# Performance work log

Measured on AMD Instinct MI355X. Metric: run time of the kernel, lower is better.

Reference implementation:

```python
import jax, jax.numpy as jnp
import numpy as np

B, T, P, D, S, R = 4, 128, 256, 512, 64, 8  # batch, window, patches, d_model, n_state, dt_rank


def setup_inputs() -> dict:
    key = jax.random.key(0)
    ks = jax.random.split(key, 8)
    sc = 0.02  # weight init scale
    return {
        "X": jax.random.normal(ks[0], (B, T, P, D), jnp.float32),
        "H0": jnp.zeros((B, P, S), jnp.float32),
        "a_hat": jax.random.normal(ks[1], (S,), jnp.float32),
        "U_w": jax.random.normal(ks[2], (S, D), jnp.float32) * sc,
        "sB_w": jax.random.normal(ks[3], (S, D), jnp.float32) * sc,
        "sB_b": jnp.zeros((S,), jnp.float32),
        "sC_w": jax.random.normal(ks[4], (S, D), jnp.float32) * sc,
        "sC_b": jnp.zeros((S,), jnp.float32),
        "sD1_w": jax.random.normal(ks[5], (R, D), jnp.float32) * sc,
        "sD1_b": jnp.zeros((R,), jnp.float32),
        "sD2_w": jax.random.normal(ks[6], (1, R), jnp.float32) * sc,
        "sD2_b": jnp.zeros((1,), jnp.float32),
        "ro_w": jax.random.normal(ks[7], (D, S), jnp.float32) * sc,
    }


def reference(X, H0, a_hat, U_w, sB_w, sB_b, sC_w, sC_b, sD1_w, sD1_b, sD2_w, sD2_b, ro_w):
    eps = 1e-12
    logA = -jnp.exp(a_hat)                                    # [S]
    # selective (input-dependent) parameters
    u = jnp.einsum('btpd,sd->btps', X, U_w)                   # [B,T,P,S]
    B_t = jnp.einsum('btpd,sd->btps', X, sB_w) + sB_b
    C_t = jnp.einsum('btpd,sd->btps', X, sC_w) + sC_b
    dt_feat = jax.nn.silu(jnp.einsum('btpd,rd->btpr', X, sD1_w) + sD1_b)
    dt = jax.nn.softplus(jnp.einsum('btpr,or->btpo', dt_feat, sD2_w) + sD2_b)  # [B,T,P,1]
    A = jnp.exp(dt * logA)                                    # [B,T,P,S] via broadcast
    b = (1.0 - A) * (B_t * u)
    # prefix-product scan: h_t = A_t*h_{t-1} + b_t  ->  h_t = P_t*(H0 + cumsum(b/P))
    Pc = jnp.cumprod(jnp.maximum(A, eps), axis=1)             # [B,T,P,S]
    invP = 1.0 / jnp.maximum(Pc, eps)
    c = jnp.cumsum(b * invP, axis=1)
    H_seq = Pc * (H0[:, None] + c)                            # [B,T,P,S]
    Y_seq = jnp.einsum('btps,ds->btpd', C_t * H_seq, ro_w)    # [B,T,P,D]
    Y_seq = Y_seq.reshape(X.shape[0], -1, X.shape[-1])        # [B, T*P, D]
    H_T = H_seq[:, -1]                                        # [B,P,S]
    return (H_seq, Y_seq, H_T)
```

## Files before the change

kernel.cpp:

```cpp
#include <hip/hip_runtime.h>
#include <hip/hip_bf16.h>
#include <math.h>

namespace {
constexpr int B_N = 4, T_N = 128, P_N = 256, D_N = 512, S_N = 64;
constexpr int NTH = 512;
constexpr int KC  = 32;
constexpr int NCH = D_N / KC;

constexpr int XS0_OFF = 0;
constexpr int WS0_OFF = 8192;
constexpr int XS1_OFF = 24576;
constexpr int WS1_OFF = 32768;
constexpr int BU_OFF  = 0;
constexpr int CH_OFF  = 16384;
constexpr int ROS0_OFF= 32768;
constexpr int ROS1_OFF= 0;
constexpr int DT_OFF  = 49152;
constexpr int LDS_BYTES = 49664;

constexpr int WIMG_ELEMS  = NCH * 256 * 32;
constexpr int ROIMG_ELEMS = 4 * 128 * 64;
}

typedef short bf16x8 __attribute__((ext_vector_type(8)));
typedef float f32x4  __attribute__((ext_vector_type(4)));

__device__ __forceinline__ unsigned short f2b(float f) {
    unsigned int x = __float_as_uint(f);
    return (unsigned short)((x + 0x7FFFu + ((x >> 16) & 1u)) >> 16);
}
__device__ __forceinline__ float b2f(unsigned short h) {
    return __uint_as_float(((unsigned int)h) << 16);
}
__device__ __forceinline__ unsigned int pk2(float lo, float hi) {
    union { __hip_bfloat162 h; unsigned int u; } cv;
    cv.h = __float22bfloat162_rn(float2{lo, hi});
    return cv.u;
}
__device__ __forceinline__ int swz32(int row, int col) {
    return row * 32 + (col ^ (((row >> 1) & 3) << 3));
}
__device__ __forceinline__ int swz64(int row, int col) {
    return row * 64 + (col ^ ((row & 7) << 3));
}
__device__ __forceinline__ void cvtstore8(unsigned short* dst, float4 a, float4 b) {
    uint4 r;
    r.x = pk2(a.x, a.y); r.y = pk2(a.z, a.w);
    r.z = pk2(b.x, b.y); r.w = pk2(b.z, b.w);
    *(uint4*)dst = r;
}
__device__ __forceinline__ void gload16(const void* g, void* l) {
    __builtin_amdgcn_global_load_lds(
        (const __attribute__((address_space(1))) unsigned int*)g,
        (__attribute__((address_space(3))) unsigned int*)l, 16, 0, 0);
}

__global__ __launch_bounds__(512) void mamba_prep(
    const float* __restrict__ U_w, const float* __restrict__ sB_w,
    const float* __restrict__ sC_w, const float* __restrict__ sD1_w,
    const float* __restrict__ ro_w,
    unsigned short* __restrict__ wImg, unsigned short* __restrict__ roImg)
{
    const int idx = blockIdx.x * 512 + threadIdx.x;
    if (idx < WIMG_ELEMS) {
        const int kc = idx >> 13, rem = idx & 8191, r = rem >> 5, c = rem & 31;
        float v = 0.0f;
        if (r < 192) {
            const int g = r >> 4, w = r & 15, tr = g % 3, sb = g / 3;
            const float* base = (tr == 0) ? U_w : (tr == 1) ? sB_w : sC_w;
            v = base[(size_t)(sb * 16 + w) * D_N + kc * KC + c];
        } else if (r < 200) {
            v = sD1_w[(size_t)(r - 192) * D_N + kc * KC + c];
        }
        wImg[kc * 8192 + swz32(r, c)] = f2b(v);
    } else if (idx < WIMG_ELEMS + ROIMG_ELEMS) {
        const int j = idx - WIMG_ELEMS;
        const int pp = j >> 13, rem = j & 8191, r = rem >> 6, c = rem & 63;
        roImg[pp * 8192 + swz64(r, c)] = f2b(ro_w[(size_t)(pp * 128 + r) * S_N + c]);
    }
}

__global__ __launch_bounds__(NTH, 4) void mamba_mfma(
    const float* __restrict__ X, const float* __restrict__ H0,
    const float* __restrict__ a_hat,
    const float* __restrict__ sB_b, const float* __restrict__ sC_b,
    const float* __restrict__ sD1_b, const float* __restrict__ sD2_w,
    const float* __restrict__ sD2_b,
    const unsigned short* __restrict__ wImg, const unsigned short* __restrict__ roImg,
    float* __restrict__ Hseq, float* __restrict__ Y, float* __restrict__ HT)
{
    __shared__ __align__(16) char smem[LDS_BYTES];
    float* DTB = (float*)(smem + DT_OFF);

    const int tid  = threadIdx.x;
    const int lane = tid & 63;
    const int wid  = tid >> 6;
    const int wm   = wid >> 2;
    const int wn   = wid & 3;
    const int l15  = lane & 15;
    const int lg   = lane >> 4;
    const int lane16 = lane * 16;
    const int b    = blockIdx.x >> 8;
    const int p    = blockIdx.x & 255;
    const char* wImgB  = (const char*)wImg;
    const char* roImgB = (const char*)roImg;

    const float la  = (tid < 64) ? -expf(a_hat[tid]) : 0.0f;
    const float h0v = (tid < 64) ? H0[((size_t)b * P_N + p) * S_N + tid] : 0.0f;

    f32x4 acc[4][3];
    f32x4 accdt;
    #pragma unroll
    for (int q = 0; q < 4; ++q) accdt[q] = 0.0f;
    #pragma unroll
    for (int mf = 0; mf < 4; ++mf)
        #pragma unroll
        for (int nf = 0; nf < 3; ++nf)
            #pragma unroll
            for (int q = 0; q < 4; ++q) acc[mf][nf][q] = 0.0f;

    const int xr = tid >> 2, xq = tid & 3;
    const float* xsrc = X + (((size_t)b * T_N + xr) * P_N + p) * D_N + xq * 8;
    const int xoff = swz32(xr, xq * 8);

    float4 xA, xB;
    {
        float4 t0 = *(const float4*)(xsrc), t1 = *(const float4*)(xsrc + 4);
        cvtstore8((unsigned short*)(smem + XS0_OFF) + xoff, t0, t1);
        gload16(wImgB + wid * 2048 + lane16,        smem + WS0_OFF + wid * 2048);
        gload16(wImgB + wid * 2048 + 1024 + lane16, smem + WS0_OFF + wid * 2048 + 1024);
        const float* n1 = xsrc + KC;
        xA = *(const float4*)(n1); xB = *(const float4*)(n1 + 4);
    }
    __syncthreads();

    const int kb = lg * 8;
    #pragma unroll 2
    for (int kc = 0; kc < NCH; ++kc) {
        unsigned short* XSc = (unsigned short*)(smem + ((kc & 1) ? XS1_OFF : XS0_OFF));
        unsigned short* WSc = (unsigned short*)(smem + ((kc & 1) ? WS1_OFF : WS0_OFF));
        char*           XSn = smem + ((kc & 1) ? XS0_OFF : XS1_OFF);
        char*           WSn = smem + ((kc & 1) ? WS0_OFF : WS1_OFF);
        if (kc + 1 < NCH) {
            cvtstore8((unsigned short*)XSn + xoff, xA, xB);
            gload16(wImgB + (kc + 1) * 16384 + wid * 2048 + lane16,        WSn + wid * 2048);
            gload16(wImgB + (kc + 1) * 16384 + wid * 2048 + 1024 + lane16, WSn + wid * 2048 + 1024);
        }
        if (kc + 2 < NCH) {
            const float* nx = xsrc + (kc + 2) * KC;
            xA = *(const float4*)(nx); xB = *(const float4*)(nx + 4);
        }
        __builtin_amdgcn_s_setprio(1);
        bf16x8 a[4];
        #pragma unroll
        for (int mf = 0; mf < 4; ++mf)
            a[mf] = *(const bf16x8*)&XSc[swz32(wm * 64 + mf * 16 + l15, kb)];
        #pragma unroll
        for (int nf = 0; nf < 3; ++nf) {
            bf16x8 bb = *(const bf16x8*)&WSc[swz32(wn * 48 + nf * 16 + l15, kb)];
            #pragma unroll
            for (int mf = 0; mf < 4; ++mf)
                acc[mf][nf] = __builtin_amdgcn_mfma_f32_16x16x32_bf16(a[mf], bb, acc[mf][nf], 0, 0, 0);
        }
        {
            bf16x8 adt = *(const bf16x8*)&XSc[swz32(wid * 16 + l15, kb)];
            bf16x8 bd  = *(const bf16x8*)&WSc[swz32(192 + l15, kb)];
            accdt = __builtin_amdgcn_mfma_f32_16x16x32_bf16(adt, bd, accdt, 0, 0, 0);
        }
        __builtin_amdgcn_s_setprio(0);
        __syncthreads();
    }

    {
        unsigned short* BU  = (unsigned short*)(smem + BU_OFF);
        unsigned short* CHB = (unsigned short*)(smem + CH_OFF);
        const int s = wn * 16 + l15;
        const float biasB = sB_b[s], biasC = sC_b[s];
        #pragma unroll
        for (int mf = 0; mf < 4; ++mf) {
            #pragma unroll
            for (int q = 0; q < 4; ++q) {
                const int t = wm * 64 + mf * 16 + lg * 4 + q;
                const float u  = acc[mf][0][q];
                const float Bv = acc[mf][1][q] + biasB;
                const float Cv = acc[mf][2][q] + biasC;
                BU[t * 64 + s]   = f2b(Bv * u);
                CHB[swz64(t, s)] = f2b(Cv);
            }
        }
    }
    {
        const float w2 = (l15 < 8) ? sD2_w[l15] : 0.0f;
        const float b1 = (l15 < 8) ? sD1_b[l15] : 0.0f;
        const float b2 = sD2_b[0];
        #pragma unroll
        for (int q = 0; q < 4; ++q) {
            float z = accdt[q] + b1;
            float w = (z / (1.0f + expf(-z))) * w2;
            w = (l15 < 8) ? w : 0.0f;
            w += __shfl_xor(w, 1);
            w += __shfl_xor(w, 2);
            w += __shfl_xor(w, 4);
            if (l15 == 0) {
                float zz = w + b2;
                DTB[wid * 16 + lg * 4 + q] = (zz > 20.0f) ? zz : log1pf(expf(zz));
            }
        }
    }
    __syncthreads();

    if (tid < 64) {
        unsigned short* BU = (unsigned short*)(smem + BU_OFF);
        const int s = tid;
        float Pcv = 1.0f, cv = 0.0f, Hv = 0.0f;
        float* hout = Hseq + ((size_t)b * T_N * P_N + p) * S_N + s;
        float bn[4], dn[4];
        #pragma unroll
        for (int q = 0; q < 4; ++q) { bn[q] = b2f(BU[q * 64 + s]); dn[q] = DTB[q]; }
        for (int t0 = 0; t0 < T_N; t0 += 4) {
            float bc[4], dc[4];
            #pragma unroll
            for (int q = 0; q < 4; ++q) { bc[q] = bn[q]; dc[q] = dn[q]; }
            if (t0 + 4 < T_N) {
                #pragma unroll
                for (int q = 0; q < 4; ++q) {
                    bn[q] = b2f(BU[(t0 + 4 + q) * 64 + s]);
                    dn[q] = DTB[t0 + 4 + q];
                }
            }
            #pragma unroll
            for (int q = 0; q < 4; ++q) {
                const int t = t0 + q;
                const float Av = expf(dc[q] * la);
                const float bv = (1.0f - Av) * bc[q];
                Pcv *= fmaxf(Av, 1e-12f);
                cv += bv * (1.0f / fmaxf(Pcv, 1e-12f));
                Hv = Pcv * (h0v + cv);
                hout[(size_t)t * P_N * S_N] = Hv;
                BU[t * 64 + s] = f2b(Hv);
            }
        }
        HT[((size_t)b * P_N + p) * S_N + s] = Hv;
    } else {
        for (int seg = wid - 1; seg < 16; seg += 7)
            gload16(roImgB + seg * 1024 + lane16, smem + ROS0_OFF + seg * 1024);
    }
    __syncthreads();

    {
        unsigned short* BU  = (unsigned short*)(smem + BU_OFF);
        unsigned short* CHB = (unsigned short*)(smem + CH_OFF);
        const int r = tid >> 2, c0 = (tid & 3) * 16;
        bf16x8 h0 = *(const bf16x8*)&BU[r * 64 + c0];
        bf16x8 h1 = *(const bf16x8*)&BU[r * 64 + c0 + 8];
        bf16x8 c8a = *(const bf16x8*)&CHB[swz64(r, c0)];
        bf16x8 c8b = *(const bf16x8*)&CHB[swz64(r, c0 + 8)];
        bf16x8 o0, o1;
        #pragma unroll
        for (int j = 0; j < 8; ++j) {
            o0[j] = (short)f2b(b2f((unsigned short)c8a[j]) * b2f((unsigned short)h0[j]));
            o1[j] = (short)f2b(b2f((unsigned short)c8b[j]) * b2f((unsigned short)h1[j]));
        }
        *(bf16x8*)&CHB[swz64(r, c0)]     = o0;
        *(bf16x8*)&CHB[swz64(r, c0 + 8)] = o1;
    }
    __syncthreads();

    bf16x8 af0[4], af1[4];
    {
        unsigned short* CHB = (unsigned short*)(smem + CH_OFF);
        #pragma unroll
        for (int mf = 0; mf < 4; ++mf) {
            af0[mf] = *(const bf16x8*)&CHB[swz64(wm * 64 + mf * 16 + l15, lg * 8)];
            af1[mf] = *(const bf16x8*)&CHB[swz64(wm * 64 + mf * 16 + l15, 32 + lg * 8)];
        }
    }

    for (int pp = 0; pp < 4; ++pp) {
        unsigned short* cur = (unsigned short*)(smem + ((pp & 1) ? ROS1_OFF : ROS0_OFF));
        char*           nxt = smem + ((pp & 1) ? ROS0_OFF : ROS1_OFF);
        if (pp < 3) {
            gload16(roImgB + (pp + 1) * 16384 + wid * 2048 + lane16,        nxt + wid * 2048);
            gload16(roImgB + (pp + 1) * 16384 + wid * 2048 + 1024 + lane16, nxt + wid * 2048 + 1024);
        }
        f32x4 yacc[4][2];
        #pragma unroll
        for (int mf = 0; mf < 4; ++mf)
            #pragma unroll
            for (int nf = 0; nf < 2; ++nf)
                #pragma unroll
                for (int q = 0; q < 4; ++q) yacc[mf][nf][q] = 0.0f;
        #pragma unroll
        for (int nf = 0; nf < 2; ++nf) {
            bf16x8 bb0 = *(const bf16x8*)&cur[swz64(wn * 32 + nf * 16 + l15, lg * 8)];
            bf16x8 bb1 = *(const bf16x8*)&cur[swz64(wn * 32 + nf * 16 + l15, 32 + lg * 8)];
            #pragma unroll
            for (int mf = 0; mf < 4; ++mf) {
                yacc[mf][nf] = __builtin_amdgcn_mfma_f32_16x16x32_bf16(bb0, af0[mf], yacc[mf][nf], 0, 0, 0);
                yacc[mf][nf] = __builtin_amdgcn_mfma_f32_16x16x32_bf16(bb1, af1[mf], yacc[mf][nf], 0, 0, 0);
            }
        }
        #pragma unroll
        for (int mf = 0; mf < 4; ++mf) {
            const int t = wm * 64 + mf * 16 + l15;
            float* ybase = Y + (((size_t)b * T_N + t) * P_N + p) * D_N;
            #pragma unroll
            for (int nf = 0; nf < 2; ++nf) {
                const int d = pp * 128 + wn * 32 + nf * 16 + lg * 4;
                *(float4*)(ybase + d) = make_float4(yacc[mf][nf][0], yacc[mf][nf][1],
                                                    yacc[mf][nf][2], yacc[mf][nf][3]);
            }
        }
        if (pp < 3) __syncthreads();
    }
}

extern "C" void kernel_launch(void* const* d_in, const int* in_sizes, int n_in,
                              void* d_out, int out_size, void* d_ws, size_t ws_size,
                              hipStream_t stream) {
    const float* X     = (const float*)d_in[0];
    const float* H0    = (const float*)d_in[1];
    const float* a_hat = (const float*)d_in[2];
    const float* U_w   = (const float*)d_in[3];
    const float* sB_w  = (const float*)d_in[4];
    const float* sB_b  = (const float*)d_in[5];
    const float* sC_w  = (const float*)d_in[6];
    const float* sC_b  = (const float*)d_in[7];
    const float* sD1_w = (const float*)d_in[8];
    const float* sD1_b = (const float*)d_in[9];
    const float* sD2_w = (const float*)d_in[10];
    const float* sD2_b = (const float*)d_in[11];
    const float* ro_w  = (const float*)d_in[12];

    float* out   = (float*)d_out;
    float* HseqP = out;
    float* YP    = out + (size_t)B_N * T_N * P_N * S_N;
    float* HTP   = YP  + (size_t)B_N * T_N * P_N * D_N;

    unsigned short* wImg  = (unsigned short*)d_ws;
    unsigned short* roImg = (unsigned short*)((char*)d_ws + 262144);

    hipLaunchKernelGGL(mamba_prep, dim3((WIMG_ELEMS + ROIMG_ELEMS) / 512), dim3(512), 0, stream,
                       U_w, sB_w, sC_w, sD1_w, ro_w, wImg, roImg);
    hipLaunchKernelGGL(mamba_mfma, dim3(B_N * P_N), dim3(NTH), 0, stream,
                       X, H0, a_hat, sB_b, sC_b, sD1_b, sD2_w, sD2_b,
                       wImg, roImg, HseqP, YP, HTP);
}
```

Before: 155.3 us.

## Stage X tiles as fp32 via async global-to-LDS loads, convert at fragment read

X chunks are now copied straight into LDS as fp32 using global_load_lds with an XOR swizzle, instead of being loaded into registers, converted to bf16 and stored. The bf16 conversion moves to fragment-read time, so each wave converts its own A fragments. The goal is to remove register staging and the conversion and store work from the load path so X loads run asynchronously like the weight loads. In exchange the LDS footprint grows from about 49KB to 66KB and conversion work is repeated per fragment read, which may add LDS traffic and ALU work inside the MFMA loop.

```diff
diff --git a/kernel.cpp b/kernel.cpp
--- a/kernel.cpp
+++ b/kernel.cpp
@@ -8,16 +8,16 @@
 constexpr int KC  = 32;
 constexpr int NCH = D_N / KC;
 
-constexpr int XS0_OFF = 0;
-constexpr int WS0_OFF = 8192;
-constexpr int XS1_OFF = 24576;
-constexpr int WS1_OFF = 32768;
+constexpr int XF0_OFF = 0;
+constexpr int XF1_OFF = 16384;
+constexpr int WS0_OFF = 32768;
+constexpr int WS1_OFF = 49152;
 constexpr int BU_OFF  = 0;
 constexpr int CH_OFF  = 16384;
 constexpr int ROS0_OFF= 32768;
-constexpr int ROS1_OFF= 0;
-constexpr int DT_OFF  = 49152;
-constexpr int LDS_BYTES = 49664;
+constexpr int ROS1_OFF= 49152;
+constexpr int DT_OFF  = 65536;
+constexpr int LDS_BYTES = 66048;
 
 constexpr int WIMG_ELEMS  = NCH * 256 * 32;
 constexpr int ROIMG_ELEMS = 4 * 128 * 64;
@@ -44,16 +44,19 @@
 __device__ __forceinline__ int swz64(int row, int col) {
     return row * 64 + (col ^ ((row & 7) << 3));
 }
-__device__ __forceinline__ void cvtstore8(unsigned short* dst, float4 a, float4 b) {
-    uint4 r;
-    r.x = pk2(a.x, a.y); r.y = pk2(a.z, a.w);
-    r.z = pk2(b.x, b.y); r.w = pk2(b.z, b.w);
-    *(uint4*)dst = r;
-}
 __device__ __forceinline__ void gload16(const void* g, void* l) {
     __builtin_amdgcn_global_load_lds(
         (const __attribute__((address_space(1))) unsigned int*)g,
         (__attribute__((address_space(3))) unsigned int*)l, 16, 0, 0);
+}
+__device__ __forceinline__ bf16x8 xfrag(const char* XF, int R, int lg) {
+    const int k = R & 7;
+    const float4 fa = *(const float4*)(XF + R * 128 + (((lg * 2)    ) ^ k) * 16);
+    const float4 fb = *(const float4*)(XF + R * 128 + (((lg * 2) + 1) ^ k) * 16);
+    union { uint4 u; bf16x8 h; } cv;
+    cv.u.x = pk2(fa.x, fa.y); cv.u.y = pk2(fa.z, fa.w);
+    cv.u.z = pk2(fb.x, fb.y); cv.u.w = pk2(fb.z, fb.w);
+    return cv.h;
 }
 
 __global__ __launch_bounds__(512) void mamba_prep(
@@ -109,6 +112,12 @@
     const float la  = (tid < 64) ? -expf(a_hat[tid]) : 0.0f;
     const float h0v = (tid < 64) ? H0[((size_t)b * P_N + p) * S_N + tid] : 0.0f;
 
+    const int ldr0 = wid * 16 + (lane >> 3);
+    const int ldr1 = ldr0 + 8;
+    const int ldu  = (lane & 7) ^ ((lane >> 3) & 7);
+    const char* srcX0 = (const char*)(X + (((size_t)b * T_N + ldr0) * P_N + p) * D_N) + ldu * 16;
+    const char* srcX1 = (const char*)(X + (((size_t)b * T_N + ldr1) * P_N + p) * D_N) + ldu * 16;
+
     f32x4 acc[4][3];
     f32x4 accdt;
     #pragma unroll
@@ -120,42 +129,30 @@
             #pragma unroll
             for (int q = 0; q < 4; ++q) acc[mf][nf][q] = 0.0f;
 
-    const int xr = tid >> 2, xq = tid & 3;
-    const float* xsrc = X + (((size_t)b * T_N + xr) * P_N + p) * D_N + xq * 8;
-    const int xoff = swz32(xr, xq * 8);
-
-    float4 xA, xB;
-    {
-        float4 t0 = *(const float4*)(xsrc), t1 = *(const float4*)(xsrc + 4);
-        cvtstore8((unsigned short*)(smem + XS0_OFF) + xoff, t0, t1);
-        gload16(wImgB + wid * 2048 + lane16,        smem + WS0_OFF + wid * 2048);
-        gload16(wImgB + wid * 2048 + 1024 + lane16, smem + WS0_OFF + wid * 2048 + 1024);
-        const float* n1 = xsrc + KC;
-        xA = *(const float4*)(n1); xB = *(const float4*)(n1 + 4);
-    }
+    gload16(srcX0, smem + XF0_OFF + wid * 2048);
+    gload16(srcX1, smem + XF0_OFF + wid * 2048 + 1024);
+    gload16(wImgB + wid * 2048 + lane16,        smem + WS0_OFF + wid * 2048);
+    gload16(wImgB + wid * 2048 + 1024 + lane16, smem + WS0_OFF + wid * 2048 + 1024);
     __syncthreads();
 
     const int kb = lg * 8;
     #pragma unroll 2
     for (int kc = 0; kc < NCH; ++kc) {
-        unsigned short* XSc = (unsigned short*)(smem + ((kc & 1) ? XS1_OFF : XS0_OFF));
+        const char*     XFc = smem + ((kc & 1) ? XF1_OFF : XF0_OFF);
         unsigned short* WSc = (unsigned short*)(smem + ((kc & 1) ? WS1_OFF : WS0_OFF));
-        char*           XSn = smem + ((kc & 1) ? XS0_OFF : XS1_OFF);
+        char*           XFn = smem + ((kc & 1) ? XF0_OFF : XF1_OFF);
         char*           WSn = smem + ((kc & 1) ? WS0_OFF : WS1_OFF);
         if (kc + 1 < NCH) {
-            cvtstore8((unsigned short*)XSn + xoff, xA, xB);
+            gload16(srcX0 + (kc + 1) * 128, XFn + wid * 2048);
+            gload16(srcX1 + (kc + 1) * 128, XFn + wid * 2048 + 1024);
             gload16(wImgB + (kc + 1) * 16384 + wid * 2048 + lane16,        WSn + wid * 2048);
             gload16(wImgB + (kc + 1) * 16384 + wid * 2048 + 1024 + lane16, WSn + wid * 2048 + 1024);
         }
-        if (kc + 2 < NCH) {
-            const float* nx = xsrc + (kc + 2) * KC;
-            xA = *(const float4*)(nx); xB = *(const float4*)(nx + 4);
-        }
         __builtin_amdgcn_s_setprio(1);
         bf16x8 a[4];
         #pragma unroll
         for (int mf = 0; mf < 4; ++mf)
-            a[mf] = *(const bf16x8*)&XSc[swz32(wm * 64 + mf * 16 + l15, kb)];
+            a[mf] = xfrag(XFc, wm * 64 + mf * 16 + l15, lg);
         #pragma unroll
         for (int nf = 0; nf < 3; ++nf) {
             bf16x8 bb = *(const bf16x8*)&WSc[swz32(wn * 48 + nf * 16 + l15, kb)];
@@ -164,7 +161,7 @@
                 acc[mf][nf] = __builtin_amdgcn_mfma_f32_16x16x32_bf16(a[mf], bb, acc[mf][nf], 0, 0, 0);
         }
         {
-            bf16x8 adt = *(const bf16x8*)&XSc[swz32(wid * 16 + l15, kb)];
+            bf16x8 adt = xfrag(XFc, wid * 16 + l15, lg);
             bf16x8 bd  = *(const bf16x8*)&WSc[swz32(192 + l15, kb)];
             accdt = __builtin_amdgcn_mfma_f32_16x16x32_bf16(adt, bd, accdt, 0, 0, 0);
         }
```

Measured after the change: 157.7 us. No clear change (+1.6%).

## Stage H_seq in LDS as fp32 and write it out with all threads vectorized

Applied to the files above, without the earlier changes.

The serial scan (64 threads) now writes H values into an fp32 LDS buffer instead of issuing strided scalar global stores per timestep. All 512 threads then emit H_seq to global memory with float4 stores and compute C*H from the fp32 values, which drops an intermediate bf16 rounding of H. The readout weight prefetch is moved after the scan, and an extra barrier is added. LDS use grows from about 49KB to 66KB, which may lower occupancy and removes the overlap of the ro prefetch with the scan.

```diff
diff --git a/kernel.cpp b/kernel.cpp
--- a/kernel.cpp
+++ b/kernel.cpp
@@ -14,10 +14,11 @@
 constexpr int WS1_OFF = 32768;
 constexpr int BU_OFF  = 0;
 constexpr int CH_OFF  = 16384;
-constexpr int ROS0_OFF= 32768;
-constexpr int ROS1_OFF= 0;
-constexpr int DT_OFF  = 49152;
-constexpr int LDS_BYTES = 49664;
+constexpr int HS_OFF  = 32768;
+constexpr int ROS0_OFF= 0;
+constexpr int ROS1_OFF= 16384;
+constexpr int DT_OFF  = 65536;
+constexpr int LDS_BYTES = 66048;
 
 constexpr int WIMG_ELEMS  = NCH * 256 * 32;
 constexpr int ROIMG_ELEMS = 4 * 128 * 64;
@@ -211,10 +212,10 @@
     __syncthreads();
 
     if (tid < 64) {
-        unsigned short* BU = (unsigned short*)(smem + BU_OFF);
+        unsigned short* BU   = (unsigned short*)(smem + BU_OFF);
+        float*          HSEQ = (float*)(smem + HS_OFF);
         const int s = tid;
         float Pcv = 1.0f, cv = 0.0f, Hv = 0.0f;
-        float* hout = Hseq + ((size_t)b * T_N * P_N + p) * S_N + s;
         float bn[4], dn[4];
         #pragma unroll
         for (int q = 0; q < 4; ++q) { bn[q] = b2f(BU[q * 64 + s]); dn[q] = DTB[q]; }
@@ -231,39 +232,55 @@
             }
             #pragma unroll
             for (int q = 0; q < 4; ++q) {
-                const int t = t0 + q;
                 const float Av = expf(dc[q] * la);
                 const float bv = (1.0f - Av) * bc[q];
                 Pcv *= fmaxf(Av, 1e-12f);
                 cv += bv * (1.0f / fmaxf(Pcv, 1e-12f));
                 Hv = Pcv * (h0v + cv);
-                hout[(size_t)t * P_N * S_N] = Hv;
-                BU[t * 64 + s] = f2b(Hv);
+                HSEQ[(t0 + q) * 64 + s] = Hv;
             }
         }
         HT[((size_t)b * P_N + p) * S_N + s] = Hv;
-    } else {
-        for (int seg = wid - 1; seg < 16; seg += 7)
-            gload16(roImgB + seg * 1024 + lane16, smem + ROS0_OFF + seg * 1024);
-    }
-    __syncthreads();
-
-    {
-        unsigned short* BU  = (unsigned short*)(smem + BU_OFF);
-        unsigned short* CHB = (unsigned short*)(smem + CH_OFF);
-        const int r = tid >> 2, c0 = (tid & 3) * 16;
-        bf16x8 h0 = *(const bf16x8*)&BU[r * 64 + c0];
-        bf16x8 h1 = *(const bf16x8*)&BU[r * 64 + c0 + 8];
-        bf16x8 c8a = *(const bf16x8*)&CHB[swz64(r, c0)];
-        bf16x8 c8b = *(const bf16x8*)&CHB[swz64(r, c0 + 8)];
-        bf16x8 o0, o1;
-        #pragma unroll
-        for (int j = 0; j < 8; ++j) {
-            o0[j] = (short)f2b(b2f((unsigned short)c8a[j]) * b2f((unsigned short)h0[j]));
-            o1[j] = (short)f2b(b2f((unsigned short)c8b[j]) * b2f((unsigned short)h1[j]));
-        }
-        *(bf16x8*)&CHB[swz64(r, c0)]     = o0;
-        *(bf16x8*)&CHB[swz64(r, c0 + 8)] = o1;
+    }
+    __syncthreads();
+
+    gload16(roImgB + wid * 2048 + lane16,        smem + ROS0_OFF + wid * 2048);
+    gload16(roImgB + wid * 2048 + 1024 + lane16, smem + ROS0_OFF + wid * 2048 + 1024);
+    {
+        float*          HSEQ = (float*)(smem + HS_OFF);
+        unsigned short* CHB  = (unsigned short*)(smem + CH_OFF);
+        const int r  = tid >> 2;
+        const int c0 = (((tid & 3) + r) & 3) * 16;
+        float4 h0 = *(const float4*)&HSEQ[r * 64 + c0];
+        float4 h1 = *(const float4*)&HSEQ[r * 64 + c0 + 4];
+        float4 h2 = *(const float4*)&HSEQ[r * 64 + c0 + 8];
+        float4 h3 = *(const float4*)&HSEQ[r * 64 + c0 + 12];
+        float* hout = Hseq + (((size_t)b * T_N + r) * P_N + p) * S_N + c0;
+        *(float4*)(hout)      = h0;
+        *(float4*)(hout + 4)  = h1;
+        *(float4*)(hout + 8)  = h2;
+        *(float4*)(hout + 12) = h3;
+        bf16x8 ca = *(const bf16x8*)&CHB[swz64(r, c0)];
+        bf16x8 cb = *(const bf16x8*)&CHB[swz64(r, c0 + 8)];
+        bf16x8 oa, ob;
+        oa[0] = (short)f2b(b2f((unsigned short)ca[0]) * h0.x);
+        oa[1] = (short)f2b(b2f((unsigned short)ca[1]) * h0.y);
+        oa[2] = (short)f2b(b2f((unsigned short)ca[2]) * h0.z);
+        oa[3] = (short)f2b(b2f((unsigned short)ca[3]) * h0.w);
+        oa[4] = (short)f2b(b2f((unsigned short)ca[4]) * h1.x);
+        oa[5] = (short)f2b(b2f((unsigned short)ca[5]) * h1.y);
+        oa[6] = (short)f2b(b2f((unsigned short)ca[6]) * h1.z);
+        oa[7] = (short)f2b(b2f((unsigned short)ca[7]) * h1.w);
+        ob[0] = (short)f2b(b2f((unsigned short)cb[0]) * h2.x);
+        ob[1] = (short)f2b(b2f((unsigned short)cb[1]) * h2.y);
+        ob[2] = (short)f2b(b2f((unsigned short)cb[2]) * h2.z);
+        ob[3] = (short)f2b(b2f((unsigned short)cb[3]) * h2.w);
+        ob[4] = (short)f2b(b2f((unsigned short)cb[4]) * h3.x);
+        ob[5] = (short)f2b(b2f((unsigned short)cb[5]) * h3.y);
+        ob[6] = (short)f2b(b2f((unsigned short)cb[6]) * h3.z);
+        ob[7] = (short)f2b(b2f((unsigned short)cb[7]) * h3.w);
+        *(bf16x8*)&CHB[swz64(r, c0)]     = oa;
+        *(bf16x8*)&CHB[swz64(r, c0 + 8)] = ob;
     }
     __syncthreads();
 
@@ -276,6 +293,7 @@
             af1[mf] = *(const bf16x8*)&CHB[swz64(wm * 64 + mf * 16 + l15, 32 + lg * 8)];
         }
     }
+    __syncthreads();
 
     for (int pp = 0; pp < 4; ++pp) {
         unsigned short* cur = (unsigned short*)(smem + ((pp & 1) ? ROS1_OFF : ROS0_OFF));
```

After: 153.0 us (median of 2 runs). About the same (-1.5%).
